# Optimization experiments

Hardware: AMD Instinct MI355X
Metric: run time of the kernel (lower is better)

Reference implementation:

```python
import jax, jax.numpy as jnp
import numpy as np

B, T, D, L, H = 16, 2048, 512, 6, 1024  # batch, seq, embed_dim, num_layers, mlp hidden (2*D)
K = D // 2  # freq bands; k = min(D//2, T//2) = 256 here
VOCAB = 256


def _ln(x, g, b, eps=1e-5):
    m = x.mean(-1, keepdims=True)
    v = ((x - m) ** 2).mean(-1, keepdims=True)
    return (x - m) / jnp.sqrt(v + eps) * g + b


def setup_inputs() -> dict:
    key = jax.random.key(0)
    ks = jax.random.split(key, 12)
    s = 0.02
    return {
        "byte_ids": jax.random.randint(ks[0], (B, T), 0, 256),
        # ByteSpectralEmbedding params
        "freq_bands": jnp.ones((K,), jnp.float32),
        "fp_w1": jax.random.normal(ks[1], (D, 2 * D), jnp.float32) * s,
        "fp_b1": jnp.zeros((2 * D,), jnp.float32),
        "fp_ln_g": jnp.ones((2 * D,), jnp.float32),
        "fp_ln_b": jnp.zeros((2 * D,), jnp.float32),
        "fp_w2": jax.random.normal(ks[2], (2 * D, D), jnp.float32) * s,
        "fp_b2": jnp.zeros((D,), jnp.float32),
        # SpectralMLPBlock params, stacked over L layers (FNet-style spectral mixing + MLP)
        "blk_ln1_g": jnp.ones((L, D), jnp.float32),
        "blk_ln1_b": jnp.zeros((L, D), jnp.float32),
        "blk_ln2_g": jnp.ones((L, D), jnp.float32),
        "blk_ln2_b": jnp.zeros((L, D), jnp.float32),
        "blk_w1": jax.random.normal(ks[3], (L, D, H), jnp.float32) * s,
        "blk_b1": jnp.zeros((L, H), jnp.float32),
        "blk_w2": jax.random.normal(ks[4], (L, H, D), jnp.float32) * s,
        "blk_b2": jnp.zeros((L, D), jnp.float32),
        # final norm + output head
        "norm_g": jnp.ones((D,), jnp.float32),
        "norm_b": jnp.zeros((D,), jnp.float32),
        "out_w": jax.random.normal(ks[5], (D, VOCAB), jnp.float32) * s,
        "out_b": jnp.zeros((VOCAB,), jnp.float32),
    }


def reference(byte_ids, freq_bands, fp_w1, fp_b1, fp_ln_g, fp_ln_b, fp_w2, fp_b2,
              blk_ln1_g, blk_ln1_b, blk_ln2_g, blk_ln2_b, blk_w1, blk_b1, blk_w2, blk_b2,
              norm_g, norm_b, out_w, out_b):
    Bc, Tc = byte_ids.shape
    k = min(D // 2, Tc // 2)
    signal = byte_ids.astype(jnp.float32) / 127.5 - 1.0          # [B,T]
    X = jnp.fft.fft(signal, axis=1)[:, :k]                        # [B,k] single FFT
    # shift theorem: FFT(roll(signal, -p))[f] = X[f] * exp(+2pi i f p / T)
    mag = jnp.abs(X) * freq_bands[:k]                             # [B,k], position-independent
    base_phase = jnp.angle(X)                                     # [B,k]
    pos = jnp.arange(Tc, dtype=jnp.float32)
    f = jnp.arange(k, dtype=jnp.float32)
    phase = base_phase[:, None, :] + (2.0 * jnp.pi / Tc) * pos[None, :, None] * f[None, None, :]  # [B,T,k]
    mag_bt = jnp.broadcast_to(mag[:, None, :], (Bc, Tc, k))
    feats = jnp.concatenate([mag_bt, jnp.sin(phase), jnp.cos(phase)], axis=-1)
    feats = feats[..., :D] if feats.shape[-1] >= D else jnp.pad(feats, ((0, 0), (0, 0), (0, D - feats.shape[-1])))
    # freq_proj: Linear -> LayerNorm -> GELU -> Linear
    h = feats @ fp_w1 + fp_b1
    h = jax.nn.gelu(_ln(h, fp_ln_g, fp_ln_b), approximate=False)
    x = h @ fp_w2 + fp_b2                                         # [B,T,D]
    # SpectralMLPBlock stack: residual FFT mixing + residual MLP
    for i in range(L):
        y = _ln(x, blk_ln1_g[i], blk_ln1_b[i])
        x = x + jnp.fft.fft(jnp.fft.fft(y, axis=-1), axis=1).real
        y = _ln(x, blk_ln2_g[i], blk_ln2_b[i])
        x = x + jax.nn.gelu(y @ blk_w1[i] + blk_b1[i], approximate=False) @ blk_w2[i] + blk_b2[i]
    x = _ln(x, norm_g, norm_b)
    return x @ out_w + out_b                                      # [B,T,256]
```

## Files before the change

### kernel.cpp

```cpp
#include <hip/hip_runtime.h>
#include <cmath>

typedef unsigned short u16;
typedef unsigned int u32;

constexpr int NB = 16;
constexpr int NT = 2048;
constexpr int ND = 512;
constexpr int NL = 6;
constexpr int NH = 1024;
constexpr int NK = 256;
constexpr int NM = NB * NT;
constexpr int NHALF = NM / 2;

constexpr float PI2 = 6.283185307179586f;

typedef short bf16x8 __attribute__((ext_vector_type(8)));
typedef float f32x4 __attribute__((ext_vector_type(4)));

__device__ __forceinline__ float gelu_exact(float v) {
    return 0.5f * v * (1.0f + erff(v * 0.70710678118654752f));
}

__device__ __forceinline__ u16 f2bf(float f) {
    union { float f; u32 u; } v; v.f = f;
    u32 r = v.u + 0x7FFFu + ((v.u >> 16) & 1u);
    return (u16)(r >> 16);
}

__device__ __forceinline__ float bf2f(u16 h) {
    union { u32 u; float f; } v; v.u = ((u32)h) << 16;
    return v.f;
}

__device__ __forceinline__ float block_sum256(float val, float* lds4) {
#pragma unroll
    for (int o = 32; o > 0; o >>= 1) val += __shfl_down(val, o);
    int lane = threadIdx.x & 63, wid = threadIdx.x >> 6;
    if (lane == 0) lds4[wid] = val;
    __syncthreads();
    float t = lds4[0] + lds4[1] + lds4[2] + lds4[3];
    __syncthreads();
    return t;
}

__device__ __forceinline__ void swz_block(int& row0, int& col0) {
    int nwg = gridDim.x * gridDim.y;
    int wg = blockIdx.x + blockIdx.y * gridDim.x;
    int L = wg;
    if ((nwg & 7) == 0) {
        int q = nwg >> 3;
        L = (wg & 7) * q + (wg >> 3);
    }
    int ncol = gridDim.y;
    row0 = (L / ncol) * 128;
    col0 = (L % ncol) * 128;
}

__global__ void dft_kernel(const int* __restrict__ bytes, const float* __restrict__ fb,
                           float* __restrict__ mag, float* __restrict__ cph,
                           float* __restrict__ sph) {
    __shared__ float lr[4], li[4];
    int b = blockIdx.x, f = blockIdx.y;
    float re = 0.f, im = 0.f;
    for (int t = threadIdx.x; t < NT; t += 256) {
        float s = (float)bytes[b * NT + t] * (1.0f / 127.5f) - 1.0f;
        int idx = (t * f) & (NT - 1);
        float a = (float)idx * (PI2 / NT);
        float sn, cs;
        sincosf(a, &sn, &cs);
        re += s * cs;
        im -= s * sn;
    }
#pragma unroll
    for (int o = 32; o > 0; o >>= 1) {
        re += __shfl_down(re, o);
        im += __shfl_down(im, o);
    }
    int lane = threadIdx.x & 63, wid = threadIdx.x >> 6;
    if (lane == 0) { lr[wid] = re; li[wid] = im; }
    __syncthreads();
    if (threadIdx.x == 0) {
        float R = lr[0] + lr[1] + lr[2] + lr[3];
        float I = li[0] + li[1] + li[2] + li[3];
        float m = sqrtf(R * R + I * I);
        mag[b * NK + f] = m * fb[f];
        float inv = (m > 0.f) ? 1.0f / m : 0.f;
        cph[b * NK + f] = (m > 0.f) ? R * inv : 1.0f;
        sph[b * NK + f] = I * inv;
    }
}

__global__ void feats_split_kernel(const float* __restrict__ mag,
                                   const float* __restrict__ cph,
                                   const float* __restrict__ sph,
                                   u16* __restrict__ hi, u16* __restrict__ lo) {
    int idx = blockIdx.x * 256 + threadIdx.x;
    int d = idx & (ND - 1);
    int m = idx >> 9;
    int b = m >> 11, t = m & (NT - 1);
    float v;
    if (d < NK) {
        v = mag[b * NK + d];
    } else {
        int f = d - NK;
        int a = (t * f) & (NT - 1);
        float sn, cs;
        sincosf((float)a * (PI2 / NT), &sn, &cs);
        v = sph[b * NK + f] * cs + cph[b * NK + f] * sn;
    }
    u16 h = f2bf(v);
    hi[idx] = h;
    lo[idx] = f2bf(v - bf2f(h));
}

template <int NV, int GELU, int OBF>
__global__ void ln_kernel(const float* __restrict__ in, const float* __restrict__ g,
                          const float* __restrict__ bta, void* __restrict__ outv) {
    __shared__ float lds4[4];
    constexpr int NE = NV / 256;
    size_t row = blockIdx.x;
    const float* p = in + row * NV;
    float v[NE];
    float sum = 0.f;
#pragma unroll
    for (int i = 0; i < NE; ++i) {
        v[i] = p[threadIdx.x + 256 * i];
        sum += v[i];
    }
    sum = block_sum256(sum, lds4);
    float mean = sum * (1.0f / NV);
    float sq = 0.f;
#pragma unroll
    for (int i = 0; i < NE; ++i) {
        float d = v[i] - mean;
        sq += d * d;
    }
    sq = block_sum256(sq, lds4);
    float inv = rsqrtf(sq * (1.0f / NV) + 1e-5f);
#pragma unroll
    for (int i = 0; i < NE; ++i) {
        int c = threadIdx.x + 256 * i;
        float r = (v[i] - mean) * inv * g[c] + bta[c];
        if (GELU) r = gelu_exact(r);
        if (OBF == 2) {
            u16* o = (u16*)outv + row * (2 * NV);
            u16 hb = f2bf(r);
            o[c] = hb;
            o[NV + c] = f2bf(r - bf2f(hb));
        } else if (OBF == 1) {
            ((u16*)outv)[row * NV + c] = f2bf(r);
        } else {
            ((float*)outv)[row * NV + c] = r;
        }
    }
}

__global__ void ln_fftd_kernel(const float* __restrict__ x, const float* __restrict__ g,
                               const float* __restrict__ bta, float* __restrict__ P,
                               int row_base) {
    __shared__ float sr[2][512], si[2][512];
    __shared__ float red[2][2];
    int sub = threadIdx.x >> 7;
    int tid = threadIdx.x & 127;
    int rlocal = blockIdx.x * 2 + sub;
    const float* p = x + ((size_t)row_base + rlocal) * ND;
    float v[4];
    float s = 0.f;
#pragma unroll
    for (int j = 0; j < 4; ++j) { v[j] = p[tid + 128 * j]; s += v[j]; }
#pragma unroll
    for (int o = 32; o > 0; o >>= 1) s += __shfl_down(s, o);
    int wv = (threadIdx.x >> 6) & 1;
    if ((threadIdx.x & 63) == 0) red[sub][wv] = s;
    __syncthreads();
    float mean = (red[sub][0] + red[sub][1]) * (1.0f / ND);
    float q = 0.f;
#pragma unroll
    for (int j = 0; j < 4; ++j) { float d = v[j] - mean; q += d * d; }
#pragma unroll
    for (int o = 32; o > 0; o >>= 1) q += __shfl_down(q, o);
    __syncthreads();
    if ((threadIdx.x & 63) == 0) red[sub][wv] = q;
    __syncthreads();
    float inv = rsqrtf((red[sub][0] + red[sub][1]) * (1.0f / ND) + 1e-5f);
#pragma unroll
    for (int j = 0; j < 4; ++j) {
        int i = tid + 128 * j;
        int r = __brev((unsigned)i) >> 23;
        sr[sub][r] = (v[j] - mean) * inv * g[i] + bta[i];
        si[sub][r] = 0.f;
    }
    __syncthreads();
    for (int len = 2; len <= 512; len <<= 1) {
        int half = len >> 1;
        for (int qq = tid; qq < 256; qq += 128) {
            int k = qq & (half - 1);
            int j = ((qq - k) << 1) + k;
            float a = -PI2 * (float)k / (float)len;
            float sn = __sinf(a), cs = __cosf(a);
            float ur = sr[sub][j], ui = si[sub][j];
            float vr = sr[sub][j + half], vi = si[sub][j + half];
            float tr = vr * cs - vi * sn;
            float ti = vr * sn + vi * cs;
            sr[sub][j] = ur + tr;
            si[sub][j] = ui + ti;
            sr[sub][j + half] = ur - tr;
            si[sub][j + half] = ui - ti;
        }
        __syncthreads();
    }
    float* out = P + (size_t)rlocal * ND;
    for (int i = tid; i < 512; i += 128)
        out[i] = (i <= 256) ? sr[sub][i] : si[sub][i - 256];
}

__global__ void transpose_bt_kernel(const float* __restrict__ P, float* __restrict__ PT) {
    __shared__ float tile[32][33];
    int b = blockIdx.z, t0 = blockIdx.x * 32, d0 = blockIdx.y * 32;
    int j = threadIdx.x & 31, i0 = threadIdx.x >> 5;
    for (int i = i0; i < 32; i += 8)
        tile[i][j] = P[((size_t)(b * NT + t0 + i)) * ND + d0 + j];
    __syncthreads();
    for (int i = i0; i < 32; i += 8)
        PT[((size_t)(b * ND + d0 + i)) * NT + t0 + j] = tile[j][i];
}

__global__ void fft_t2048_kernel(const float* __restrict__ PT, float* __restrict__ Mt) {
    __shared__ float sr[2048], si[2048];
    int b = blockIdx.x;
    int d = blockIdx.y;
    const float* zr = PT + ((size_t)(b * ND + d)) * NT;
    const float* zi = PT + ((size_t)(b * ND + 256 + d)) * NT;
    bool has_im = (d != 0) && (d != 256);
    for (int t = threadIdx.x; t < 2048; t += 256) {
        int r = __brev((unsigned)t) >> 21;
        sr[r] = zr[t];
        si[r] = has_im ? zi[t] : 0.f;
    }
    __syncthreads();
    for (int len = 2; len <= 2048; len <<= 1) {
        int half = len >> 1;
        for (int q = threadIdx.x; q < 1024; q += 256) {
            int k = q & (half - 1);
            int j = ((q - k) << 1) + k;
            float a = -PI2 * (float)k / (float)len;
            float sn = __sinf(a), cs = __cosf(a);
            float ur = sr[j], ui = si[j];
            float vr = sr[j + half], vi = si[j + half];
            float tr = vr * cs - vi * sn;
            float ti = vr * sn + vi * cs;
            sr[j] = ur + tr;
            si[j] = ui + ti;
            sr[j + half] = ur - tr;
            si[j + half] = ui - ti;
        }
        __syncthreads();
    }
    float* m0 = Mt + ((size_t)(b * ND + d)) * NT;
    for (int t = threadIdx.x; t < 2048; t += 256) m0[t] = sr[t];
    if (has_im) {
        float* m1 = Mt + ((size_t)(b * ND + (512 - d))) * NT;
        for (int t = threadIdx.x; t < 2048; t += 256) m1[t] = sr[(2048 - t) & 2047];
    }
}

__global__ void add_transpose_kernel(const float* __restrict__ Mt, float* __restrict__ x) {
    __shared__ float tile[32][33];
    int b = blockIdx.z, t0 = blockIdx.x * 32, d0 = blockIdx.y * 32;
    int j = threadIdx.x & 31, i0 = threadIdx.x >> 5;
    for (int i = i0; i < 32; i += 8)
        tile[i][j] = Mt[((size_t)(b * ND + d0 + i)) * NT + t0 + j];
    __syncthreads();
    for (int i = i0; i < 32; i += 8) {
        size_t xi = ((size_t)(b * NT + t0 + i)) * ND + d0 + j;
        x[xi] += tile[j][i];
    }
}

__global__ void wconv_kernel(const float* __restrict__ W, u16* __restrict__ Wt,
                             int K, int N) {
    __shared__ float tile[32][33];
    size_t moff = (size_t)blockIdx.z * K * N;
    int n0 = blockIdx.x * 32, k0 = blockIdx.y * 32;
    int j = threadIdx.x & 31, i0 = threadIdx.x >> 5;
    for (int i = i0; i < 32; i += 8)
        tile[i][j] = W[moff + (size_t)(k0 + i) * N + n0 + j];
    __syncthreads();
    for (int i = i0; i < 32; i += 8)
        Wt[moff + (size_t)(n0 + i) * K + k0 + j] = f2bf(tile[j][i]);
}

template <int GELU, int ACC, int OBF, int ADDB>
__global__ __launch_bounds__(256) void mfma_gemm(
    const u16* __restrict__ A, int lda, const u16* __restrict__ Wt,
    const float* __restrict__ bias, void* __restrict__ Cv, int Kd, int Nd) {
    __shared__ __align__(16) u16 Al[3][4096];
    __shared__ __align__(16) u16 Bl[3][4096];
    int tid = threadIdx.x;
    int row0, col0;
    swz_block(row0, col0);
    int lane = tid & 63, w = tid >> 6;
    int wr = w >> 1, wc = w & 1;
    int kg = lane >> 4, ln16 = lane & 15;

    f32x4 acc[4][4] = {};

    auto stage = [&](int buf, int t) {
        int k0 = t << 5;
#pragma unroll
        for (int i = 0; i < 2; ++i) {
            int s = i * 256 + tid;
            int skg = s >> 7, r = s & 127;
            const u16* ga = A + (size_t)(row0 + r) * lda + k0 + skg * 8;
            __builtin_amdgcn_global_load_lds(
                (const __attribute__((address_space(1))) void*)ga,
                (__attribute__((address_space(3))) void*)&Al[buf][s * 8], 16, 0, 0);
            const u16* gb = Wt + (size_t)(col0 + r) * Kd + k0 + skg * 8;
            __builtin_amdgcn_global_load_lds(
                (const __attribute__((address_space(1))) void*)gb,
                (__attribute__((address_space(3))) void*)&Bl[buf][s * 8], 16, 0, 0);
        }
    };
    auto compute = [&](int buf) {
        bf16x8 af[4], bfr[4];
#pragma unroll
        for (int mi = 0; mi < 4; ++mi)
            af[mi] = *(const bf16x8*)&Al[buf][(kg * 128 + wr * 64 + mi * 16 + ln16) * 8];
#pragma unroll
        for (int ni = 0; ni < 4; ++ni)
            bfr[ni] = *(const bf16x8*)&Bl[buf][(kg * 128 + wc * 64 + ni * 16 + ln16) * 8];
#pragma unroll
        for (int mi = 0; mi < 4; ++mi)
#pragma unroll
            for (int ni = 0; ni < 4; ++ni)
                acc[mi][ni] = __builtin_amdgcn_mfma_f32_16x16x32_bf16(
                    af[mi], bfr[ni], acc[mi][ni], 0, 0, 0);
    };

    int nt = Kd >> 5;
    stage(0, 0);
    stage(1, 1);
    for (int t = 0; t < nt; ++t) {
        if (t + 1 < nt) asm volatile("s_waitcnt vmcnt(4)" ::: "memory");
        else            asm volatile("s_waitcnt vmcnt(0)" ::: "memory");
        __builtin_amdgcn_sched_barrier(0);
        __builtin_amdgcn_s_barrier();
        __builtin_amdgcn_sched_barrier(0);
        if (t + 2 < nt) stage((t + 2) % 3, t + 2);
        compute(t % 3);
    }

#pragma unroll
    for (int mi = 0; mi < 4; ++mi) {
#pragma unroll
        for (int ni = 0; ni < 4; ++ni) {
            int col = col0 + wc * 64 + ni * 16 + ln16;
            float bv = ADDB ? bias[col] : 0.f;
#pragma unroll
            for (int j = 0; j < 4; ++j) {
                int row = row0 + wr * 64 + mi * 16 + kg * 4 + j;
                float v = acc[mi][ni][j] + bv;
                if (GELU) v = gelu_exact(v);
                size_t o = (size_t)row * Nd + col;
                if (OBF) {
                    ((u16*)Cv)[o] = f2bf(v);
                } else {
                    float* C = (float*)Cv;
                    if (ACC) v += C[o];
                    C[o] = v;
                }
            }
        }
    }
}

__global__ __launch_bounds__(256) void mfma_gemm2(
    const u16* __restrict__ Ahi, const u16* __restrict__ Alo, int lda,
    const u16* __restrict__ Wt, const float* __restrict__ bias,
    float* __restrict__ C, int Kd, int Nd) {
    __shared__ __align__(16) u16 Ah[3][4096];
    __shared__ __align__(16) u16 Al2[3][4096];
    __shared__ __align__(16) u16 Bl[3][4096];
    int tid = threadIdx.x;
    int row0, col0;
    swz_block(row0, col0);
    int lane = tid & 63, w = tid >> 6;
    int wr = w >> 1, wc = w & 1;
    int kg = lane >> 4, ln16 = lane & 15;

    f32x4 acc[4][4] = {};

    auto stage = [&](int buf, int t) {
        int k0 = t << 5;
#pragma unroll
        for (int i = 0; i < 2; ++i) {
            int s = i * 256 + tid;
            int skg = s >> 7, r = s & 127;
            size_t aoff = (size_t)(row0 + r) * lda + k0 + skg * 8;
            __builtin_amdgcn_global_load_lds(
                (const __attribute__((address_space(1))) void*)(Ahi + aoff),
                (__attribute__((address_space(3))) void*)&Ah[buf][s * 8], 16, 0, 0);
            __builtin_amdgcn_global_load_lds(
                (const __attribute__((address_space(1))) void*)(Alo + aoff),
                (__attribute__((address_space(3))) void*)&Al2[buf][s * 8], 16, 0, 0);
            const u16* gb = Wt + (size_t)(col0 + r) * Kd + k0 + skg * 8;
            __builtin_amdgcn_global_load_lds(
                (const __attribute__((address_space(1))) void*)gb,
                (__attribute__((address_space(3))) void*)&Bl[buf][s * 8], 16, 0, 0);
        }
    };
    auto compute = [&](int buf) {
        bf16x8 ah[4], al[4], bfr[4];
#pragma unroll
        for (int mi = 0; mi < 4; ++mi) {
            int sl = (kg * 128 + wr * 64 + mi * 16 + ln16) * 8;
            ah[mi] = *(const bf16x8*)&Ah[buf][sl];
            al[mi] = *(const bf16x8*)&Al2[buf][sl];
        }
#pragma unroll
        for (int ni = 0; ni < 4; ++ni)
            bfr[ni] = *(const bf16x8*)&Bl[buf][(kg * 128 + wc * 64 + ni * 16 + ln16) * 8];
#pragma unroll
        for (int mi = 0; mi < 4; ++mi)
#pragma unroll
            for (int ni = 0; ni < 4; ++ni) {
                acc[mi][ni] = __builtin_amdgcn_mfma_f32_16x16x32_bf16(
                    ah[mi], bfr[ni], acc[mi][ni], 0, 0, 0);
                acc[mi][ni] = __builtin_amdgcn_mfma_f32_16x16x32_bf16(
                    al[mi], bfr[ni], acc[mi][ni], 0, 0, 0);
            }
    };

    int nt = Kd >> 5;
    stage(0, 0);
    stage(1, 1);
    for (int t = 0; t < nt; ++t) {
        if (t + 1 < nt) asm volatile("s_waitcnt vmcnt(6)" ::: "memory");
        else            asm volatile("s_waitcnt vmcnt(0)" ::: "memory");
        __builtin_amdgcn_sched_barrier(0);
        __builtin_amdgcn_s_barrier();
        __builtin_amdgcn_sched_barrier(0);
        if (t + 2 < nt) stage((t + 2) % 3, t + 2);
        compute(t % 3);
    }

#pragma unroll
    for (int mi = 0; mi < 4; ++mi) {
#pragma unroll
        for (int ni = 0; ni < 4; ++ni) {
            int col = col0 + wc * 64 + ni * 16 + ln16;
            float bv = bias[col];
#pragma unroll
            for (int j = 0; j < 4; ++j) {
                int row = row0 + wr * 64 + mi * 16 + kg * 4 + j;
                C[(size_t)row * Nd + col] = acc[mi][ni][j] + bv;
            }
        }
    }
}

extern "C" void kernel_launch(void* const* d_in, const int* in_sizes, int n_in,
                              void* d_out, int out_size, void* d_ws, size_t ws_size,
                              hipStream_t stream) {
    const int* byte_ids     = (const int*)d_in[0];
    const float* freq_bands = (const float*)d_in[1];
    const float* fp_w1   = (const float*)d_in[2];
    const float* fp_b1   = (const float*)d_in[3];
    const float* fp_ln_g = (const float*)d_in[4];
    const float* fp_ln_b = (const float*)d_in[5];
    const float* fp_w2   = (const float*)d_in[6];
    const float* fp_b2   = (const float*)d_in[7];
    const float* blk_ln1_g = (const float*)d_in[8];
    const float* blk_ln1_b = (const float*)d_in[9];
    const float* blk_ln2_g = (const float*)d_in[10];
    const float* blk_ln2_b = (const float*)d_in[11];
    const float* blk_w1  = (const float*)d_in[12];
    const float* blk_b1  = (const float*)d_in[13];
    const float* blk_w2  = (const float*)d_in[14];
    const float* blk_b2  = (const float*)d_in[15];
    const float* norm_g  = (const float*)d_in[16];
    const float* norm_b  = (const float*)d_in[17];
    const float* out_w   = (const float*)d_in[18];
    const float* out_b   = (const float*)d_in[19];
    float* out = (float*)d_out;
    char* base = (char*)d_ws;
    const size_t MB = 1048576;

    u16* fhi     = (u16*)base;
    u16* flo     = (u16*)(base + 32 * MB);
    float* xA    = (float*)base;
    float* hfp   = (float*)(base + 64 * MB);
    u16* h2      = (u16*)hfp;
    float* Zbuf  = (float*)(base + 64 * MB);
    float* PTbuf = (float*)(base + 96 * MB);
    float* Mtbuf = Zbuf;
    u16* hmlp    = (u16*)(base + 64 * MB);
    u16* ybf     = (u16*)(base + 128 * MB);
    u16* wbase   = (u16*)(base + 160 * MB);
    u16* blkw1t  = wbase;
    u16* blkw2t  = wbase + 3145728;
    u16* outwt   = wbase + 6291456;
    u16* fpw1t   = (u16*)d_out;
    u16* fpw2t   = (u16*)((char*)d_out + 1 * MB);
    float* mag   = (float*)((char*)d_out + 2 * MB);
    float* cph   = mag + NB * NK;
    float* sph   = cph + NB * NK;

    dft_kernel<<<dim3(NB, NK), 256, 0, stream>>>(byte_ids, freq_bands, mag, cph, sph);
    feats_split_kernel<<<(NM * ND) / 256, 256, 0, stream>>>(mag, cph, sph, fhi, flo);
    wconv_kernel<<<dim3(NH / 32, ND / 32, 1), 256, 0, stream>>>(fp_w1, fpw1t, ND, NH);
    wconv_kernel<<<dim3(ND / 32, NH / 32, 1), 256, 0, stream>>>(fp_w2, fpw2t, NH, ND);

    mfma_gemm2<<<dim3(NM / 128, NH / 128), 256, 0, stream>>>(
        fhi, flo, ND, fpw1t, fp_b1, hfp, ND, NH);
    ln_kernel<NH, 1, 2><<<NM, 256, 0, stream>>>(hfp, fp_ln_g, fp_ln_b, h2);
    mfma_gemm2<<<dim3(NM / 128, ND / 128), 256, 0, stream>>>(
        h2, h2 + NH, 2 * NH, fpw2t, fp_b2, xA, NH, ND);

    wconv_kernel<<<dim3(NH / 32, ND / 32, NL), 256, 0, stream>>>(blk_w1, blkw1t, ND, NH);
    wconv_kernel<<<dim3(ND / 32, NH / 32, NL), 256, 0, stream>>>(blk_w2, blkw2t, NH, ND);
    wconv_kernel<<<dim3(256 / 32, ND / 32, 1), 256, 0, stream>>>(out_w, outwt, ND, 256);

    for (int l = 0; l < NL; ++l) {
        for (int hh = 0; hh < 2; ++hh) {
            int row_base = hh * NHALF;
            ln_fftd_kernel<<<NHALF / 2, 256, 0, stream>>>(
                xA, blk_ln1_g + l * ND, blk_ln1_b + l * ND, Zbuf, row_base);
            transpose_bt_kernel<<<dim3(NT / 32, ND / 32, 8), 256, 0, stream>>>(Zbuf, PTbuf);
            fft_t2048_kernel<<<dim3(8, 257), 256, 0, stream>>>(PTbuf, Mtbuf);
            add_transpose_kernel<<<dim3(NT / 32, ND / 32, 8), 256, 0, stream>>>(
                Mtbuf, xA + (size_t)row_base * ND);
        }
        ln_kernel<ND, 0, 1><<<NM, 256, 0, stream>>>(
            xA, blk_ln2_g + l * ND, blk_ln2_b + l * ND, ybf);
        mfma_gemm<1, 0, 1, 1><<<dim3(NM / 128, NH / 128), 256, 0, stream>>>(
            ybf, ND, blkw1t + (size_t)l * ND * NH, blk_b1 + l * NH, hmlp, ND, NH);
        mfma_gemm<0, 1, 0, 1><<<dim3(NM / 128, ND / 128), 256, 0, stream>>>(
            hmlp, NH, blkw2t + (size_t)l * ND * NH, blk_b2 + l * ND, xA, NH, ND);
    }

    ln_kernel<ND, 0, 1><<<NM, 256, 0, stream>>>(xA, norm_g, norm_b, ybf);
    mfma_gemm<0, 0, 0, 1><<<dim3(NM / 128, 256 / 128), 256, 0, stream>>>(
        ybf, ND, outwt, out_b, out, ND, 256);
}
```

Baseline: 3.226 ms.

## Precompute FFT twiddle table and switch GEMM to double-buffered LDS pipeline

Adds a small kernel that precomputes a per-stage twiddle table in global memory, which both FFT kernels now load instead of evaluating sin/cos for every butterfly. Separately, the bf16 MFMA GEMM drops from a three-stage LDS ring with explicit vmcnt waits to a simpler two-buffer scheme with __syncthreads. The table lookup trades transcendental ALU work for cached global loads. The GEMM change lowers LDS use but may expose more load latency, since compute now waits on a full barrier every K-tile.

```diff
diff --git a/kernel.cpp b/kernel.cpp
--- a/kernel.cpp
+++ b/kernel.cpp
@@ -55,6 +55,17 @@
     int ncol = gridDim.y;
     row0 = (L / ncol) * 128;
     col0 = (L % ncol) * 128;
+}
+
+__global__ void twiddle_kernel(float2* __restrict__ tw) {
+    int idx = blockIdx.x * 256 + threadIdx.x;
+    if (idx < 2047) {
+        u32 v = idx + 1;
+        u32 h = 1u << (31 - __clz(v));
+        u32 k = v - h;
+        float a = -(float)M_PI * (float)k / (float)h;
+        tw[idx] = make_float2(cosf(a), sinf(a));
+    }
 }
 
 __global__ void dft_kernel(const int* __restrict__ bytes, const float* __restrict__ fb,
@@ -158,7 +169,7 @@
 
 __global__ void ln_fftd_kernel(const float* __restrict__ x, const float* __restrict__ g,
                                const float* __restrict__ bta, float* __restrict__ P,
-                               int row_base) {
+                               int row_base, const float2* __restrict__ twid) {
     __shared__ float sr[2][512], si[2][512];
     __shared__ float red[2][2];
     int sub = threadIdx.x >> 7;
@@ -197,8 +208,8 @@
         for (int qq = tid; qq < 256; qq += 128) {
             int k = qq & (half - 1);
             int j = ((qq - k) << 1) + k;
-            float a = -PI2 * (float)k / (float)len;
-            float sn = __sinf(a), cs = __cosf(a);
+            float2 tw = twid[(half - 1) + k];
+            float cs = tw.x, sn = tw.y;
             float ur = sr[sub][j], ui = si[sub][j];
             float vr = sr[sub][j + half], vi = si[sub][j + half];
             float tr = vr * cs - vi * sn;
@@ -226,7 +237,8 @@
         PT[((size_t)(b * ND + d0 + i)) * NT + t0 + j] = tile[j][i];
 }
 
-__global__ void fft_t2048_kernel(const float* __restrict__ PT, float* __restrict__ Mt) {
+__global__ void fft_t2048_kernel(const float* __restrict__ PT, float* __restrict__ Mt,
+                                 const float2* __restrict__ twid) {
     __shared__ float sr[2048], si[2048];
     int b = blockIdx.x;
     int d = blockIdx.y;
@@ -244,8 +256,8 @@
         for (int q = threadIdx.x; q < 1024; q += 256) {
             int k = q & (half - 1);
             int j = ((q - k) << 1) + k;
-            float a = -PI2 * (float)k / (float)len;
-            float sn = __sinf(a), cs = __cosf(a);
+            float2 tw = twid[(half - 1) + k];
+            float cs = tw.x, sn = tw.y;
             float ur = sr[j], ui = si[j];
             float vr = sr[j + half], vi = si[j + half];
             float tr = vr * cs - vi * sn;
@@ -295,8 +307,8 @@
 __global__ __launch_bounds__(256) void mfma_gemm(
     const u16* __restrict__ A, int lda, const u16* __restrict__ Wt,
     const float* __restrict__ bias, void* __restrict__ Cv, int Kd, int Nd) {
-    __shared__ __align__(16) u16 Al[3][4096];
-    __shared__ __align__(16) u16 Bl[3][4096];
+    __shared__ __align__(16) u16 Al[2][4096];
+    __shared__ __align__(16) u16 Bl[2][4096];
     int tid = threadIdx.x;
     int row0, col0;
     swz_block(row0, col0);
@@ -340,16 +352,15 @@
 
     int nt = Kd >> 5;
     stage(0, 0);
-    stage(1, 1);
-    for (int t = 0; t < nt; ++t) {
-        if (t + 1 < nt) asm volatile("s_waitcnt vmcnt(4)" ::: "memory");
-        else            asm volatile("s_waitcnt vmcnt(0)" ::: "memory");
-        __builtin_amdgcn_sched_barrier(0);
-        __builtin_amdgcn_s_barrier();
-        __builtin_amdgcn_sched_barrier(0);
-        if (t + 2 < nt) stage((t + 2) % 3, t + 2);
-        compute(t % 3);
-    }
+    __syncthreads();
+    int cur = 0;
+    for (int t = 1; t < nt; ++t) {
+        stage(cur ^ 1, t);
+        compute(cur);
+        __syncthreads();
+        cur ^= 1;
+    }
+    compute(cur);
 
 #pragma unroll
     for (int mi = 0; mi < 4; ++mi) {
@@ -506,6 +517,9 @@
     float* mag   = (float*)((char*)d_out + 2 * MB);
     float* cph   = mag + NB * NK;
     float* sph   = cph + NB * NK;
+    float2* twid = (float2*)((char*)d_out + 4 * MB);
+
+    twiddle_kernel<<<8, 256, 0, stream>>>(twid);
 
     dft_kernel<<<dim3(NB, NK), 256, 0, stream>>>(byte_ids, freq_bands, mag, cph, sph);
     feats_split_kernel<<<(NM * ND) / 256, 256, 0, stream>>>(mag, cph, sph, fhi, flo);
@@ -526,9 +540,9 @@
         for (int hh = 0; hh < 2; ++hh) {
             int row_base = hh * NHALF;
             ln_fftd_kernel<<<NHALF / 2, 256, 0, stream>>>(
-                xA, blk_ln1_g + l * ND, blk_ln1_b + l * ND, Zbuf, row_base);
+                xA, blk_ln1_g + l * ND, blk_ln1_b + l * ND, Zbuf, row_base, twid);
             transpose_bt_kernel<<<dim3(NT / 32, ND / 32, 8), 256, 0, stream>>>(Zbuf, PTbuf);
-            fft_t2048_kernel<<<dim3(8, 257), 256, 0, stream>>>(PTbuf, Mtbuf);
+            fft_t2048_kernel<<<dim3(8, 257), 256, 0, stream>>>(PTbuf, Mtbuf, twid);
             add_transpose_kernel<<<dim3(NT / 32, ND / 32, 8), 256, 0, stream>>>(
                 Mtbuf, xA + (size_t)row_base * ND);
         }
```

Measured after the change: 3.038 ms. 5.8% less time.
